# Kernel tuning notes

Measured on AMD Instinct MI355X. Metric: run time of the kernel, lower is better.

Reference implementation:

```python
import jax, jax.numpy as jnp
import numpy as np

B, T, L, H, W, D = 16, 4096, 4, 128, 128, 32  # batch, points, views, plane HxW, c_dim
MAX_DIM = 0.55


def _linear_init(key, fan_in, fan_out):
    k1, k2 = jax.random.split(key)
    bound = 1.0 / np.sqrt(fan_in)
    Wm = jax.random.uniform(k1, (fan_in, fan_out), minval=-bound, maxval=bound, dtype=jnp.float32)
    b = jax.random.uniform(k2, (fan_out,), minval=-bound, maxval=bound, dtype=jnp.float32)
    return Wm, b


def setup_inputs() -> dict:
    key = jax.random.key(0)
    ks = jax.random.split(key, 10)
    p = jax.random.uniform(ks[0], (B, T, 3), dtype=jnp.float32, minval=-0.5, maxval=0.5)
    z = jax.random.normal(ks[1], (B, 128), dtype=jnp.float32)
    c = jax.random.normal(ks[2], (B, L, H, W, D), dtype=jnp.float32)
    C_mat = jax.random.normal(ks[3], (B, L, 4, 3), dtype=jnp.float32)
    fc_p_W, fc_p_b = _linear_init(ks[4], 3, D)
    # 5 ResnetBlockFC blocks, each with fc_0 and fc_1 (D->D)
    W0s, b0s, W1s, b1s = [], [], [], []
    for i in range(5):
        kk = jax.random.split(ks[5 + (i % 4)], 2 * (i + 1))
        w0, bb0 = _linear_init(jax.random.fold_in(key, 100 + i), D, D)
        w1, bb1 = _linear_init(jax.random.fold_in(key, 200 + i), D, D)
        W0s.append(w0); b0s.append(bb0); W1s.append(w1); b1s.append(bb1)
    blocks_W0 = jnp.stack(W0s); blocks_b0 = jnp.stack(b0s)
    blocks_W1 = jnp.stack(W1s); blocks_b1 = jnp.stack(b1s)
    fc_out_W, fc_out_b = _linear_init(ks[9], D, 1)
    return {
        'p': p, 'z': z, 'c': c, 'C_mat': C_mat,
        'fc_p_W': fc_p_W, 'fc_p_b': fc_p_b,
        'blocks_W0': blocks_W0, 'blocks_b0': blocks_b0,
        'blocks_W1': blocks_W1, 'blocks_b1': blocks_b1,
        'fc_out_W': fc_out_W, 'fc_out_b': fc_out_b,
    }


def bilinear_interpolation(p, net, C_mat):
    # p: [B,T,3]; net: [B,L,H,W,D]; C_mat: [B,L,4,3]
    Bb, Ll, Hh, Ww, Dd = net.shape
    interval = 2.0 / (Hh - 1)
    # project points with all views at once: C[:, l, :3] @ p^T, vectorized over l
    proj = jnp.einsum('blij,btj->blti', C_mat[:, :, :3, :], p / MAX_DIM)  # [B,L,T,3]
    proj = proj / (C_mat[:, :, 3, 0] + 0.05)[:, :, None, None]
    xy = (proj[..., :2] + 1.0) / interval  # [B,L,T,2]
    xy = jnp.where(xy >= Hh - 1, Hh - 1 - 0.1, xy)
    xy = jnp.where(xy < 0, 0.0, xy)
    xg, yg = xy[..., 0], xy[..., 1]  # [B,L,T]
    # torch.round and jnp.round both round half-to-even
    xl = jnp.round(xg - 0.5); xr = jnp.round(xg + 0.5)
    yl = jnp.round(yg - 0.5); yh = jnp.round(yg + 0.5)
    xi_l = xl.astype(jnp.int32); xi_r = xr.astype(jnp.int32)
    yi_l = yl.astype(jnp.int32); yi_h = yh.astype(jnp.int32)
    bi = jnp.arange(Bb)[:, None, None]
    li = jnp.arange(Ll)[None, :, None]
    f11 = net[bi, li, xi_l, yi_l]  # [B,L,T,D]
    f12 = net[bi, li, xi_r, yi_l]
    f21 = net[bi, li, xi_l, yi_h]
    f22 = net[bi, li, xi_r, yi_h]
    dx = (xr - xg)[..., None]
    dy = (yh - yg)[..., None]
    feat = f11 * dx * dy + f12 * (1 - dx) * dy + f21 * dx * (1 - dy) + f22 * (1 - dx) * (1 - dy)
    return jnp.sum(feat, axis=1)  # sum over views -> [B,T,D]


def resnet_block(x, W0, b0, W1, b1):
    # ResnetBlockFC(size_in == size_out): x + fc_1(relu(fc_0(relu(x))))
    h = jax.nn.relu(x) @ W0 + b0
    dx = jax.nn.relu(h) @ W1 + b1
    return x + dx


def reference(p, z, c, C_mat, fc_p_W, fc_p_b, blocks_W0, blocks_b0, blocks_W1, blocks_b1, fc_out_W, fc_out_b):
    cf = bilinear_interpolation(p, c, C_mat)  # [B,T,D]
    net = p @ fc_p_W + fc_p_b  # [B,T,D]
    net = net + cf
    net = resnet_block(net, blocks_W0[0], blocks_b0[0], blocks_W1[0], blocks_b1[0])
    for i in range(1, 5):
        net = net + cf
        net = resnet_block(net, blocks_W0[i], blocks_b0[i], blocks_W1[i], blocks_b1[i])
    out = jax.nn.relu(net) @ fc_out_W + fc_out_b  # [B,T,1]
    return out[..., 0]
```

## Files before the change

### kernel.cpp

```cpp
#include <hip/hip_runtime.h>


#define LL 4
#define HH 128
#define WW 128
#define DD 32
#define NPT 65536

__device__ __forceinline__ float bcast(float v, int srclane) {
    return __int_as_float(__builtin_amdgcn_readlane(__float_as_int(v), srclane));
}

__global__ __launch_bounds__(256) void gather_kernel(
    const float* __restrict__ p,
    const float* __restrict__ c,
    const float* __restrict__ Cmat,
    float4* __restrict__ cf_ws)
{
    const int tid = blockIdx.x * blockDim.x + threadIdx.x;
    const int t  = tid >> 3;
    const int dg = tid & 7;
    const int b  = t >> 12;

    const float* pp = p + (size_t)t * 3;
    const float pm0 = pp[0] / 0.55f;
    const float pm1 = pp[1] / 0.55f;
    const float pm2 = pp[2] / 0.55f;

    const float interval = (float)(2.0 / 127.0);

    float4 acc = make_float4(0.f, 0.f, 0.f, 0.f);

    #pragma unroll
    for (int l = 0; l < LL; ++l) {
        const float* cm = Cmat + (size_t)(b * LL + l) * 12;
        const float c00 = cm[0], c01 = cm[1], c02 = cm[2];
        const float c10 = cm[3], c11 = cm[4], c12 = cm[5];
        const float c30 = cm[9];

        float pr0 = c00 * pm0 + c01 * pm1 + c02 * pm2;
        float pr1 = c10 * pm0 + c11 * pm1 + c12 * pm2;
        const float denom = c30 + 0.05f;
        pr0 = pr0 / denom;
        pr1 = pr1 / denom;

        float xg = (pr0 + 1.0f) / interval;
        float yg = (pr1 + 1.0f) / interval;
        xg = (xg >= 127.0f) ? 126.9f : xg;
        xg = (xg < 0.0f)    ? 0.0f   : xg;
        yg = (yg >= 127.0f) ? 126.9f : yg;
        yg = (yg < 0.0f)    ? 0.0f   : yg;

        const float xl = rintf(xg - 0.5f);
        const float xr = rintf(xg + 0.5f);
        const float yl = rintf(yg - 0.5f);
        const float yh = rintf(yg + 0.5f);
        const int xil = (int)xl, xir = (int)xr, yil = (int)yl, yih = (int)yh;

        const float dx = xr - xg;
        const float dy = yh - yg;
        const float w11 = dx * dy;
        const float w12 = (1.0f - dx) * dy;
        const float w21 = dx * (1.0f - dy);
        const float w22 = (1.0f - dx) * (1.0f - dy);

        const float* plane = c + (size_t)(b * LL + l) * (HH * WW * DD);
        const int doff = dg * 4;
        const float4 a  = *(const float4*)(plane + ((size_t)xil * WW + yil) * DD + doff);
        const float4 e  = *(const float4*)(plane + ((size_t)xir * WW + yil) * DD + doff);
        const float4 g  = *(const float4*)(plane + ((size_t)xil * WW + yih) * DD + doff);
        const float4 d4 = *(const float4*)(plane + ((size_t)xir * WW + yih) * DD + doff);

        acc.x += w11 * a.x + w12 * e.x + w21 * g.x + w22 * d4.x;
        acc.y += w11 * a.y + w12 * e.y + w21 * g.y + w22 * d4.y;
        acc.z += w11 * a.z + w12 * e.z + w21 * g.z + w22 * d4.z;
        acc.w += w11 * a.w + w12 * e.w + w21 * g.w + w22 * d4.w;
    }

    cf_ws[tid] = acc;
}

__global__ __launch_bounds__(256) void mlp_kernel(
    const float* __restrict__ p,
    const float* __restrict__ cf_ws,
    const float* __restrict__ fc_p_W,
    const float* __restrict__ fc_p_b,
    const float* __restrict__ W0,
    const float* __restrict__ b0,
    const float* __restrict__ W1,
    const float* __restrict__ b1,
    const float* __restrict__ fc_out_W,
    const float* __restrict__ fc_out_b,
    float* __restrict__ out)
{
    const int t    = blockIdx.x * blockDim.x + threadIdx.x;
    const int lane = threadIdx.x & 63;
    const int j32  = lane & 31;

    const float* pp = p + (size_t)t * 3;
    const float px = pp[0], py = pp[1], pz = pp[2];

    float cf[DD];
    const float4* cfv = (const float4*)(cf_ws + (size_t)t * DD);
    #pragma unroll
    for (int q = 0; q < DD / 4; ++q) {
        const float4 v = cfv[q];
        cf[4*q+0] = v.x; cf[4*q+1] = v.y; cf[4*q+2] = v.z; cf[4*q+3] = v.w;
    }

    const float vpb  = fc_p_b[j32];
    const float vpw0 = fc_p_W[j32];
    const float vpw1 = fc_p_W[DD + j32];
    const float vpw2 = fc_p_W[2 * DD + j32];

    float net[DD];
    #pragma unroll
    for (int j = 0; j < DD; ++j) {
        net[j] = bcast(vpb, j) + px * bcast(vpw0, j) + py * bcast(vpw1, j)
               + pz * bcast(vpw2, j) + cf[j];
    }

    float h[DD];
    for (int s = 0; s < 5; ++s) {
        const float* Ws0 = W0 + (size_t)s * DD * DD;
        const float* Ws1 = W1 + (size_t)s * DD * DD;
        float wa[16], wb[16];
        #pragma unroll
        for (int r = 0; r < 16; ++r) wa[r] = Ws0[r * 64 + lane];
        #pragma unroll
        for (int r = 0; r < 16; ++r) wb[r] = Ws1[r * 64 + lane];
        const float vb0 = b0[s * DD + j32];
        const float vb1 = b1[s * DD + j32];

        if (s > 0) {
            #pragma unroll
            for (int j = 0; j < DD; ++j) net[j] += cf[j];
        }

        float r0[DD];
        #pragma unroll
        for (int j = 0; j < DD; ++j) r0[j] = fmaxf(net[j], 0.0f);
        #pragma unroll
        for (int j = 0; j < DD; ++j) h[j] = bcast(vb0, j);
        #pragma unroll
        for (int k = 0; k < DD; ++k) {
            const float xk = r0[k];
            #pragma unroll
            for (int j = 0; j < DD; ++j) {
                const int f = k * DD + j;
                h[j] += xk * bcast(wa[f >> 6], f & 63);
            }
        }

        #pragma unroll
        for (int j = 0; j < DD; ++j) net[j] += bcast(vb1, j);
        #pragma unroll
        for (int j = 0; j < DD; ++j) r0[j] = fmaxf(h[j], 0.0f);
        #pragma unroll
        for (int k = 0; k < DD; ++k) {
            const float xk = r0[k];
            #pragma unroll
            for (int j = 0; j < DD; ++j) {
                const int f = k * DD + j;
                net[j] += xk * bcast(wb[f >> 6], f & 63);
            }
        }
    }

    const float vwo = fc_out_W[j32];
    float o = fc_out_b[0];
    #pragma unroll
    for (int k = 0; k < DD; ++k) o += fmaxf(net[k], 0.0f) * bcast(vwo, k);
    out[t] = o;
}

__global__ __launch_bounds__(256) void decoder_fused_kernel(
    const float* __restrict__ p,
    const float* __restrict__ c,
    const float* __restrict__ Cmat,
    const float* __restrict__ fc_p_W,
    const float* __restrict__ fc_p_b,
    const float* __restrict__ W0,
    const float* __restrict__ b0,
    const float* __restrict__ W1,
    const float* __restrict__ b1,
    const float* __restrict__ fc_out_W,
    const float* __restrict__ fc_out_b,
    float* __restrict__ out)
{
    const int t = blockIdx.x * blockDim.x + threadIdx.x;
    const int b = t >> 12;

    const float* pp = p + (size_t)t * 3;
    const float px = pp[0], py = pp[1], pz = pp[2];
    const float pm0 = px / 0.55f, pm1 = py / 0.55f, pm2 = pz / 0.55f;

    float cf[DD];
    #pragma unroll
    for (int j = 0; j < DD; ++j) cf[j] = 0.0f;
    const float interval = (float)(2.0 / 127.0);

    #pragma unroll
    for (int l = 0; l < LL; ++l) {
        const float* cm = Cmat + (size_t)(b * LL + l) * 12;
        float pr0 = cm[0]*pm0 + cm[1]*pm1 + cm[2]*pm2;
        float pr1 = cm[3]*pm0 + cm[4]*pm1 + cm[5]*pm2;
        const float denom = cm[9] + 0.05f;
        pr0 /= denom; pr1 /= denom;
        float xg = (pr0 + 1.0f) / interval;
        float yg = (pr1 + 1.0f) / interval;
        xg = (xg >= 127.0f) ? 126.9f : xg; xg = (xg < 0.0f) ? 0.0f : xg;
        yg = (yg >= 127.0f) ? 126.9f : yg; yg = (yg < 0.0f) ? 0.0f : yg;
        const float xl = rintf(xg - 0.5f), xr = rintf(xg + 0.5f);
        const float yl = rintf(yg - 0.5f), yh = rintf(yg + 0.5f);
        const int xil = (int)xl, xir = (int)xr, yil = (int)yl, yih = (int)yh;
        const float dx = xr - xg, dy = yh - yg;
        const float w11 = dx*dy, w12 = (1.f-dx)*dy, w21 = dx*(1.f-dy), w22 = (1.f-dx)*(1.f-dy);
        const float* plane = c + (size_t)(b * LL + l) * (HH * WW * DD);
        const float4* f11 = (const float4*)(plane + ((size_t)xil * WW + yil) * DD);
        const float4* f12 = (const float4*)(plane + ((size_t)xir * WW + yil) * DD);
        const float4* f21 = (const float4*)(plane + ((size_t)xil * WW + yih) * DD);
        const float4* f22 = (const float4*)(plane + ((size_t)xir * WW + yih) * DD);
        #pragma unroll
        for (int q = 0; q < DD / 4; ++q) {
            const float4 a = f11[q], e = f12[q], g = f21[q], d4 = f22[q];
            cf[4*q+0] += w11*a.x + w12*e.x + w21*g.x + w22*d4.x;
            cf[4*q+1] += w11*a.y + w12*e.y + w21*g.y + w22*d4.y;
            cf[4*q+2] += w11*a.z + w12*e.z + w21*g.z + w22*d4.z;
            cf[4*q+3] += w11*a.w + w12*e.w + w21*g.w + w22*d4.w;
        }
    }

    float net[DD];
    #pragma unroll
    for (int j = 0; j < DD; ++j)
        net[j] = fc_p_b[j] + px*fc_p_W[j] + py*fc_p_W[DD+j] + pz*fc_p_W[2*DD+j] + cf[j];

    for (int s = 0; s < 5; ++s) {
        if (s > 0) {
            #pragma unroll
            for (int j = 0; j < DD; ++j) net[j] += cf[j];
        }
        const float* w0 = W0 + (size_t)s * DD * DD;
        const float* w1 = W1 + (size_t)s * DD * DD;
        float h[DD];
        #pragma unroll
        for (int j = 0; j < DD; ++j) h[j] = b0[s * DD + j];
        #pragma unroll 4
        for (int k = 0; k < DD; ++k) {
            const float xk = fmaxf(net[k], 0.0f);
            #pragma unroll
            for (int j = 0; j < DD; ++j) h[j] += xk * w0[k * DD + j];
        }
        #pragma unroll
        for (int j = 0; j < DD; ++j) net[j] += b1[s * DD + j];
        #pragma unroll 4
        for (int k = 0; k < DD; ++k) {
            const float hk = fmaxf(h[k], 0.0f);
            #pragma unroll
            for (int j = 0; j < DD; ++j) net[j] += hk * w1[k * DD + j];
        }
    }

    float o = fc_out_b[0];
    #pragma unroll
    for (int k = 0; k < DD; ++k) o += fmaxf(net[k], 0.0f) * fc_out_W[k];
    out[t] = o;
}

extern "C" void kernel_launch(void* const* d_in, const int* in_sizes, int n_in,
                              void* d_out, int out_size, void* d_ws, size_t ws_size,
                              hipStream_t stream) {
    const float* p        = (const float*)d_in[0];
    const float* c        = (const float*)d_in[2];
    const float* Cmat     = (const float*)d_in[3];
    const float* fc_p_W   = (const float*)d_in[4];
    const float* fc_p_b   = (const float*)d_in[5];
    const float* W0       = (const float*)d_in[6];
    const float* b0       = (const float*)d_in[7];
    const float* W1       = (const float*)d_in[8];
    const float* b1       = (const float*)d_in[9];
    const float* fc_out_W = (const float*)d_in[10];
    const float* fc_out_b = (const float*)d_in[11];
    float* out = (float*)d_out;

    const size_t cf_bytes = (size_t)NPT * DD * 4;

    if (ws_size >= cf_bytes) {
        float* cf_ws = (float*)d_ws;
        gather_kernel<<<(NPT * 8) / 256, 256, 0, stream>>>(p, c, Cmat, (float4*)cf_ws);
        mlp_kernel<<<NPT / 256, 256, 0, stream>>>(p, cf_ws, fc_p_W, fc_p_b,
                                                  W0, b0, W1, b1, fc_out_W, fc_out_b, out);
    } else {
        decoder_fused_kernel<<<NPT / 256, 256, 0, stream>>>(p, c, Cmat, fc_p_W, fc_p_b,
                                                            W0, b0, W1, b1, fc_out_W, fc_out_b, out);
    }
}
```

Baseline: 238.7 us.

## Run the residual MLP on bf16 MFMA with 16-point tiles per wave

Replaces the per-thread scalar MLP, which used readlane broadcasts of the weights, with a wave-level formulation. Each wave handles 16 points, and the 32x32 layers run on mfma_f32_16x16x32_bf16 with weights pre-packed to bf16 in registers. Activations are passed through shared memory to re-layout them into A fragments between layers. The intent is to cut the large VALU cost of the dense layers, at the price of bf16 rounding of weights and activations, extra barriers, and four times as many blocks.

Measured after the change: 211.9 us. 1.13x faster.

```diff
diff --git a/kernel.cpp b/kernel.cpp
--- a/kernel.cpp
+++ b/kernel.cpp
@@ -1,4 +1,5 @@
 #include <hip/hip_runtime.h>
+#include <hip/hip_bf16.h>
 
 
 #define LL 4
@@ -7,8 +8,17 @@
 #define DD 32
 #define NPT 65536
 
-__device__ __forceinline__ float bcast(float v, int srclane) {
-    return __int_as_float(__builtin_amdgcn_readlane(__float_as_int(v), srclane));
+typedef __attribute__((ext_vector_type(8))) short bf16x8t;
+typedef __attribute__((ext_vector_type(4))) float f32x4;
+
+union ABfrag { bf16x8t v; unsigned u[4]; };
+
+__device__ __forceinline__ unsigned pk2(float a, float b) {
+    __hip_bfloat16 ha = __float2bfloat16(a);
+    __hip_bfloat16 hb = __float2bfloat16(b);
+    unsigned short ua = *reinterpret_cast<unsigned short*>(&ha);
+    unsigned short ub = *reinterpret_cast<unsigned short*>(&hb);
+    return (unsigned)ua | ((unsigned)ub << 16);
 }
 
 __global__ __launch_bounds__(256) void gather_kernel(
@@ -28,7 +38,6 @@
     const float pm2 = pp[2] / 0.55f;
 
     const float interval = (float)(2.0 / 127.0);
-
     float4 acc = make_float4(0.f, 0.f, 0.f, 0.f);
 
     #pragma unroll
@@ -80,7 +89,7 @@
     cf_ws[tid] = acc;
 }
 
-__global__ __launch_bounds__(256) void mlp_kernel(
+__global__ __launch_bounds__(256) void mlp_mfma_kernel(
     const float* __restrict__ p,
     const float* __restrict__ cf_ws,
     const float* __restrict__ fc_p_W,
@@ -93,85 +102,139 @@
     const float* __restrict__ fc_out_b,
     float* __restrict__ out)
 {
-    const int t    = blockIdx.x * blockDim.x + threadIdx.x;
+    __shared__ float xb[4][16][36];
+
     const int lane = threadIdx.x & 63;
-    const int j32  = lane & 31;
-
-    const float* pp = p + (size_t)t * 3;
-    const float px = pp[0], py = pp[1], pz = pp[2];
-
-    float cf[DD];
-    const float4* cfv = (const float4*)(cf_ws + (size_t)t * DD);
-    #pragma unroll
-    for (int q = 0; q < DD / 4; ++q) {
-        const float4 v = cfv[q];
-        cf[4*q+0] = v.x; cf[4*q+1] = v.y; cf[4*q+2] = v.z; cf[4*q+3] = v.w;
-    }
-
-    const float vpb  = fc_p_b[j32];
-    const float vpw0 = fc_p_W[j32];
-    const float vpw1 = fc_p_W[DD + j32];
-    const float vpw2 = fc_p_W[2 * DD + j32];
-
-    float net[DD];
-    #pragma unroll
-    for (int j = 0; j < DD; ++j) {
-        net[j] = bcast(vpb, j) + px * bcast(vpw0, j) + py * bcast(vpw1, j)
-               + pz * bcast(vpw2, j) + cf[j];
-    }
-
-    float h[DD];
+    const int wv   = threadIdx.x >> 6;
+    const int cch  = lane & 15;
+    const int q    = lane >> 4;
+    const int tpt  = (blockIdx.x * 4 + wv) * 16;
+
+    float (*myxb)[36] = xb[wv];
+
+    unsigned wB[5][2][2][4];
+    #pragma unroll
     for (int s = 0; s < 5; ++s) {
-        const float* Ws0 = W0 + (size_t)s * DD * DD;
-        const float* Ws1 = W1 + (size_t)s * DD * DD;
-        float wa[16], wb[16];
-        #pragma unroll
-        for (int r = 0; r < 16; ++r) wa[r] = Ws0[r * 64 + lane];
-        #pragma unroll
-        for (int r = 0; r < 16; ++r) wb[r] = Ws1[r * 64 + lane];
-        const float vb0 = b0[s * DD + j32];
-        const float vb1 = b1[s * DD + j32];
-
+        #pragma unroll
+        for (int m = 0; m < 2; ++m) {
+            const float* Wm = (m ? W1 : W0) + s * DD * DD;
+            #pragma unroll
+            for (int tile = 0; tile < 2; ++tile) {
+                const float* base = Wm + tile * 16 + cch;
+                #pragma unroll
+                for (int i = 0; i < 4; ++i) {
+                    const float wlo = base[(8 * q + 2 * i)     * DD];
+                    const float whi = base[(8 * q + 2 * i + 1) * DD];
+                    wB[s][m][tile][i] = pk2(wlo, whi);
+                }
+            }
+        }
+    }
+    float bc0[5][2], bc1[5][2];
+    #pragma unroll
+    for (int s = 0; s < 5; ++s) {
+        bc0[s][0] = b0[s * DD + cch];
+        bc0[s][1] = b0[s * DD + 16 + cch];
+        bc1[s][0] = b1[s * DD + cch];
+        bc1[s][1] = b1[s * DD + 16 + cch];
+    }
+    const float fpb0 = fc_p_b[cch],      fpb1 = fc_p_b[16 + cch];
+    const float fw00 = fc_p_W[cch],      fw01 = fc_p_W[16 + cch];
+    const float fw10 = fc_p_W[DD + cch], fw11 = fc_p_W[DD + 16 + cch];
+    const float fw20 = fc_p_W[2*DD + cch], fw21 = fc_p_W[2*DD + 16 + cch];
+
+    f32x4 net0, net1, cf0, cf1;
+    #pragma unroll
+    for (int r = 0; r < 4; ++r) {
+        const int pt = tpt + q * 4 + r;
+        cf0[r] = cf_ws[(size_t)pt * DD + cch];
+        cf1[r] = cf_ws[(size_t)pt * DD + 16 + cch];
+        const float* pp = p + (size_t)pt * 3;
+        const float px = pp[0], py = pp[1], pz = pp[2];
+        net0[r] = fpb0 + px * fw00 + py * fw10 + pz * fw20 + cf0[r];
+        net1[r] = fpb1 + px * fw01 + py * fw11 + pz * fw21 + cf1[r];
+    }
+
+    #pragma unroll
+    for (int s = 0; s < 5; ++s) {
         if (s > 0) {
             #pragma unroll
-            for (int j = 0; j < DD; ++j) net[j] += cf[j];
-        }
-
-        float r0[DD];
-        #pragma unroll
-        for (int j = 0; j < DD; ++j) r0[j] = fmaxf(net[j], 0.0f);
-        #pragma unroll
-        for (int j = 0; j < DD; ++j) h[j] = bcast(vb0, j);
-        #pragma unroll
-        for (int k = 0; k < DD; ++k) {
-            const float xk = r0[k];
-            #pragma unroll
-            for (int j = 0; j < DD; ++j) {
-                const int f = k * DD + j;
-                h[j] += xk * bcast(wa[f >> 6], f & 63);
-            }
-        }
-
-        #pragma unroll
-        for (int j = 0; j < DD; ++j) net[j] += bcast(vb1, j);
-        #pragma unroll
-        for (int j = 0; j < DD; ++j) r0[j] = fmaxf(h[j], 0.0f);
-        #pragma unroll
-        for (int k = 0; k < DD; ++k) {
-            const float xk = r0[k];
-            #pragma unroll
-            for (int j = 0; j < DD; ++j) {
-                const int f = k * DD + j;
-                net[j] += xk * bcast(wb[f >> 6], f & 63);
-            }
-        }
-    }
-
-    const float vwo = fc_out_W[j32];
-    float o = fc_out_b[0];
-    #pragma unroll
-    for (int k = 0; k < DD; ++k) o += fmaxf(net[k], 0.0f) * bcast(vwo, k);
-    out[t] = o;
+            for (int r = 0; r < 4; ++r) { net0[r] += cf0[r]; net1[r] += cf1[r]; }
+        }
+
+        #pragma unroll
+        for (int r = 0; r < 4; ++r) {
+            myxb[q * 4 + r][cch]      = fmaxf(net0[r], 0.0f);
+            myxb[q * 4 + r][16 + cch] = fmaxf(net1[r], 0.0f);
+        }
+        __syncthreads();
+        ABfrag A1;
+        {
+            const float* row = myxb[cch] + 8 * q;
+            const f32x4 alo = *(const f32x4*)(row);
+            const f32x4 ahi = *(const f32x4*)(row + 4);
+            A1.u[0] = pk2(alo[0], alo[1]);
+            A1.u[1] = pk2(alo[2], alo[3]);
+            A1.u[2] = pk2(ahi[0], ahi[1]);
+            A1.u[3] = pk2(ahi[2], ahi[3]);
+        }
+        __syncthreads();
+
+        f32x4 h0 = { bc0[s][0], bc0[s][0], bc0[s][0], bc0[s][0] };
+        f32x4 h1 = { bc0[s][1], bc0[s][1], bc0[s][1], bc0[s][1] };
+        {
+            ABfrag B0a, B0b;
+            #pragma unroll
+            for (int i = 0; i < 4; ++i) { B0a.u[i] = wB[s][0][0][i]; B0b.u[i] = wB[s][0][1][i]; }
+            h0 = __builtin_amdgcn_mfma_f32_16x16x32_bf16(A1.v, B0a.v, h0, 0, 0, 0);
+            h1 = __builtin_amdgcn_mfma_f32_16x16x32_bf16(A1.v, B0b.v, h1, 0, 0, 0);
+        }
+
+        #pragma unroll
+        for (int r = 0; r < 4; ++r) {
+            myxb[q * 4 + r][cch]      = fmaxf(h0[r], 0.0f);
+            myxb[q * 4 + r][16 + cch] = fmaxf(h1[r], 0.0f);
+        }
+        __syncthreads();
+        ABfrag A2;
+        {
+            const float* row = myxb[cch] + 8 * q;
+            const f32x4 alo = *(const f32x4*)(row);
+            const f32x4 ahi = *(const f32x4*)(row + 4);
+            A2.u[0] = pk2(alo[0], alo[1]);
+            A2.u[1] = pk2(alo[2], alo[3]);
+            A2.u[2] = pk2(ahi[0], ahi[1]);
+            A2.u[3] = pk2(ahi[2], ahi[3]);
+        }
+        __syncthreads();
+
+        #pragma unroll
+        for (int r = 0; r < 4; ++r) { net0[r] += bc1[s][0]; net1[r] += bc1[s][1]; }
+        {
+            ABfrag B1a, B1b;
+            #pragma unroll
+            for (int i = 0; i < 4; ++i) { B1a.u[i] = wB[s][1][0][i]; B1b.u[i] = wB[s][1][1][i]; }
+            net0 = __builtin_amdgcn_mfma_f32_16x16x32_bf16(A2.v, B1a.v, net0, 0, 0, 0);
+            net1 = __builtin_amdgcn_mfma_f32_16x16x32_bf16(A2.v, B1b.v, net1, 0, 0, 0);
+        }
+    }
+
+    const float wo0 = fc_out_W[cch];
+    const float wo1 = fc_out_W[16 + cch];
+    float acc[4];
+    #pragma unroll
+    for (int r = 0; r < 4; ++r)
+        acc[r] = fmaxf(net0[r], 0.0f) * wo0 + fmaxf(net1[r], 0.0f) * wo1;
+    #pragma unroll
+    for (int m = 1; m < 16; m <<= 1) {
+        #pragma unroll
+        for (int r = 0; r < 4; ++r) acc[r] += __shfl_xor(acc[r], m, 64);
+    }
+    if (cch == 0) {
+        const float ob = fc_out_b[0];
+        #pragma unroll
+        for (int r = 0; r < 4; ++r) out[tpt + q * 4 + r] = acc[r] + ob;
+    }
 }
 
 __global__ __launch_bounds__(256) void decoder_fused_kernel(
@@ -222,12 +285,12 @@
         const float4* f21 = (const float4*)(plane + ((size_t)xil * WW + yih) * DD);
         const float4* f22 = (const float4*)(plane + ((size_t)xir * WW + yih) * DD);
         #pragma unroll
-        for (int q = 0; q < DD / 4; ++q) {
-            const float4 a = f11[q], e = f12[q], g = f21[q], d4 = f22[q];
-            cf[4*q+0] += w11*a.x + w12*e.x + w21*g.x + w22*d4.x;
-            cf[4*q+1] += w11*a.y + w12*e.y + w21*g.y + w22*d4.y;
-            cf[4*q+2] += w11*a.z + w12*e.z + w21*g.z + w22*d4.z;
-            cf[4*q+3] += w11*a.w + w12*e.w + w21*g.w + w22*d4.w;
+        for (int qq = 0; qq < DD / 4; ++qq) {
+            const float4 a = f11[qq], e = f12[qq], g = f21[qq], d4 = f22[qq];
+            cf[4*qq+0] += w11*a.x + w12*e.x + w21*g.x + w22*d4.x;
+            cf[4*qq+1] += w11*a.y + w12*e.y + w21*g.y + w22*d4.y;
+            cf[4*qq+2] += w11*a.z + w12*e.z + w21*g.z + w22*d4.z;
+            cf[4*qq+3] += w11*a.w + w12*e.w + w21*g.w + w22*d4.w;
         }
     }
 
@@ -289,8 +352,8 @@
     if (ws_size >= cf_bytes) {
         float* cf_ws = (float*)d_ws;
         gather_kernel<<<(NPT * 8) / 256, 256, 0, stream>>>(p, c, Cmat, (float4*)cf_ws);
-        mlp_kernel<<<NPT / 256, 256, 0, stream>>>(p, cf_ws, fc_p_W, fc_p_b,
-                                                  W0, b0, W1, b1, fc_out_W, fc_out_b, out);
+        mlp_mfma_kernel<<<NPT / 64, 256, 0, stream>>>(p, cf_ws, fc_p_W, fc_p_b,
+                                                      W0, b0, W1, b1, fc_out_W, fc_out_b, out);
     } else {
         decoder_fused_kernel<<<NPT / 256, 256, 0, stream>>>(p, c, Cmat, fc_p_W, fc_p_b,
                                                             W0, b0, W1, b1, fc_out_W, fc_out_b, out);
```
